# Kernel tuning notes

Measured on AMD Instinct MI355X. Metric: run time of the kernel, lower is better.

Reference implementation:

```python
import jax, jax.numpy as jnp
import numpy as np

B = 16384      # games
BS = 19        # board size
N2 = BS * BS   # 361
G = 8          # groups per board
S = 4          # stones per group
R = B * G      # total groups
K = R * S      # total stones
M = N2         # hash history length (H*W*history_factor)
I32MIN = np.iinfo(np.int32).min
I32MAX = np.iinfo(np.int32).max
NEG = jnp.float32(-1e9)


def setup_inputs() -> dict:
    key = jax.random.key(0)
    ks = jax.random.split(key, 10)
    logits = jax.random.normal(ks[0], (B, BS, BS), dtype=jnp.float32)
    legal_mask = jax.random.uniform(ks[1], (B, BS, BS)) < 0.7
    current_player = jax.random.randint(ks[2], (B,), 0, 2, dtype=jnp.int32)
    current_hash = jax.random.randint(ks[3], (B,), 0, I32MAX, dtype=jnp.int32)
    hash_history = jax.random.randint(ks[4], (B, M), 0, I32MAX, dtype=jnp.int32)
    move_count = jax.random.randint(ks[5], (B,), 0, M, dtype=jnp.int32)
    ZposT = jax.random.randint(ks[6], (3, N2), 0, I32MAX, dtype=jnp.int32)
    stone_global_index = jax.random.randint(ks[7], (K,), 0, N2, dtype=jnp.int32)
    stone_global_pointer = jnp.arange(R + 1, dtype=jnp.int32) * S          # CSR: stones per group
    group_global_pointer_per_board = jnp.arange(B + 1, dtype=jnp.int32) * G  # CSR: groups per board
    cap_idx = jax.random.randint(ks[8], (B, N2, 4), 0, G, dtype=jnp.int32)
    cap_on = jax.random.uniform(ks[9], (B, N2, 4)) < 0.05
    captured_group_local_index = jnp.where(cap_on, cap_idx, jnp.int32(-1))
    return {
        "logits": logits,
        "legal_mask": legal_mask,
        "current_player": current_player,
        "current_hash": current_hash,
        "hash_history": hash_history,
        "move_count": move_count,
        "ZposT": ZposT,
        "stone_global_index": stone_global_index,
        "stone_global_pointer": stone_global_pointer,
        "group_global_pointer_per_board": group_global_pointer_per_board,
        "captured_group_local_index": captured_group_local_index,
    }


def reference(logits, legal_mask, current_player, current_hash, hash_history,
              move_count, ZposT, stone_global_index, stone_global_pointer,
              group_global_pointer_per_board, captured_group_local_index):
    Bn, H, W = legal_mask.shape
    Rn = stone_global_pointer.shape[0] - 1
    Kn = stone_global_index.shape[0]
    z_empty, z_black, z_white = ZposT[0], ZposT[1], ZposT[2]

    # Placement delta: empty -> current player's stone, for every candidate point. (B, N2)
    placement_delta = z_empty[None, :] ^ jnp.where(
        (current_player == 0)[:, None], z_black[None, :], z_white[None, :])

    # Map each group -> board, each stone -> group (CSR expansion).
    groups_per_board = group_global_pointer_per_board[1:] - group_global_pointer_per_board[:-1]
    group_board = jnp.repeat(jnp.arange(Bn, dtype=jnp.int32), groups_per_board,
                             total_repeat_length=Rn)
    stones_per_group = stone_global_pointer[1:] - stone_global_pointer[:-1]
    group_for_stone = jnp.repeat(jnp.arange(Rn, dtype=jnp.int32), stones_per_group,
                                 total_repeat_length=Kn)
    stone_board = group_board[group_for_stone]

    # Per-stone removal delta: opponent stone -> empty.
    opp_for_stone = (1 - current_player)[stone_board]           # (K,)
    si = stone_global_index.astype(jnp.int32)
    z_opp = ZposT[1 + opp_for_stone, si]
    per_stone_delta = z_opp ^ z_empty[si]                        # (K,) int32

    # Segmented XOR reduction over each group's stones via XOR prefix scan.
    prefix = jax.lax.associative_scan(jnp.bitwise_xor, per_stone_delta)
    start = stone_global_pointer[:-1]
    end = stone_global_pointer[1:]
    end_val = prefix[jnp.clip(end - 1, 0)]
    start_val = jnp.where(start > 0, prefix[jnp.clip(start - 1, 0)], jnp.int32(0))
    group_xor = end_val ^ start_val                              # (R,) per-group removal delta

    # Gather capture deltas for up to 4 captured neighbor groups per candidate move.
    offs = group_global_pointer_per_board[:-1][:, None, None]    # (B,1,1)
    flat_ids = jnp.clip(captured_group_local_index, 0) + offs    # (B,N2,4)
    cap_vals = jnp.where(captured_group_local_index >= 0, group_xor[flat_ids], jnp.int32(0))
    capture_delta = cap_vals[..., 0] ^ cap_vals[..., 1] ^ cap_vals[..., 2] ^ cap_vals[..., 3]

    candidate = current_hash[:, None] ^ placement_delta ^ capture_delta  # (B, N2)

    # Super-ko repeat detection against hash history (mask, sort, searchsorted).
    Mh = hash_history.shape[1]
    valid = jnp.arange(Mh, dtype=jnp.int32)[None, :] < jnp.minimum(move_count, Mh)[:, None]
    masked_hist = jnp.where(valid, hash_history, jnp.int32(I32MIN))
    sorted_hist = jnp.sort(masked_hist, axis=1)
    idx = jnp.clip(
        jax.vmap(lambda h, c: jnp.searchsorted(h, c, side='right'))(sorted_hist, candidate) - 1,
        0)
    found = jnp.take_along_axis(sorted_hist, idx, axis=1)
    repeat = (found == candidate).reshape(Bn, H, W)

    final_mask = legal_mask & ~repeat
    return jnp.where(final_mask, logits, NEG)
```

## Files before the change

### kernel.cpp

```cpp
#include <hip/hip_runtime.h>
#include <stdint.h>

#define N2 361
#define BMW 512u
#define EMPTY 0x80000000u
#define NEGV -998244352.0f

__global__ __launch_bounds__(256) void k_groups(
    const int* __restrict__ current_player,
    const int* __restrict__ ZposT,
    const int* __restrict__ stone_global_index,
    const int* __restrict__ stone_global_pointer,
    unsigned*  __restrict__ gx_out,
    const void* __restrict__ legal_raw,
    unsigned*  __restrict__ fmt_out,
    int packed_bits, int Rn)
{
    const int r = blockIdx.x * 256 + threadIdx.x;

    if (blockIdx.x == 0 && threadIdx.x < 64) {
        const int lane = threadIdx.x;
        const unsigned* lwd = (const unsigned*)legal_raw;
        const unsigned dv0 = lwd[lane];
        const unsigned dv1 = (lane < 27) ? lwd[64 + lane] : 0u;
        auto classify = [](unsigned v) -> unsigned {
            unsigned f = 0;
            #pragma unroll
            for (int j = 0; j < 4; ++j) {
                const unsigned bv = (v >> (8 * j)) & 0xFFu;
                if (bv > 1u) f |= 1u;
                if (j != 0 && bv != 0u) f |= 2u;
            }
            const unsigned x = v & 0xFFFFu, y = v >> 16;
            if ((x && x != 0x3F80u) || (y && y != 0x3F80u)) f |= 4u;
            if (x == 0x3F80u) f |= 8u;
            return f;
        };
        unsigned fcl = classify(dv0);
        if (lane < 27) fcl |= classify(dv1);
        unsigned fa = 0;
        fa |= __ballot(fcl & 1u) ? 1u : 0u;
        fa |= __ballot(fcl & 2u) ? 2u : 0u;
        fa |= __ballot(fcl & 4u) ? 4u : 0u;
        fa |= __ballot(fcl & 8u) ? 8u : 0u;
        unsigned fmt;
        if (packed_bits) fmt = 4u;
        else if (!(fa & 1u)) fmt = (fa & 2u) ? 1u : 0u;
        else if (!(fa & 4u)) fmt = (fa & 8u) ? 2u : 0u;
        else fmt = 1u;
        if (lane == 0) fmt_out[0] = fmt;
    }

    if (r < Rn) {
        const int sp0 = stone_global_pointer[r];
        const int sp1 = stone_global_pointer[r + 1];
        const int b   = r >> 3;
        const int cp  = current_player[b];
        const int opprow = (2 - cp) * N2;
        unsigned x = 0u;
        for (int k = sp0; k < sp1; ++k) {
            const int si = stone_global_index[k];
            x ^= (unsigned)ZposT[opprow + si] ^ (unsigned)ZposT[si];
        }
        gx_out[r] = x;
    }
}

__device__ __forceinline__ unsigned sel8(uint4 a, uint4 b, unsigned i) {
    const unsigned r01 = (i & 1u) ? a.y : a.x;
    const unsigned r23 = (i & 1u) ? a.w : a.z;
    const unsigned r45 = (i & 1u) ? b.y : b.x;
    const unsigned r67 = (i & 1u) ? b.w : b.z;
    const unsigned r03 = (i & 2u) ? r23 : r01;
    const unsigned r47 = (i & 2u) ? r67 : r45;
    return (i & 4u) ? r47 : r03;
}

__global__ __launch_bounds__(384) void k_cand(
    const int* __restrict__ current_hash,
    const int* __restrict__ current_player,
    const int* __restrict__ ZposT,
    const int4* __restrict__ captured4,
    const unsigned* __restrict__ gx_ws,
    unsigned* __restrict__ cand_out)
{
    const int b = blockIdx.x;
    const int t = threadIdx.x;
    if (t >= N2) return;
    const unsigned ch = (unsigned)current_hash[b];
    const int cp = current_player[b];
    const uint4 ga = *(const uint4*)(gx_ws + b * 8);
    const uint4 gb = *(const uint4*)(gx_ws + b * 8 + 4);
    const size_t q = (size_t)b * N2 + t;
    const int4 c = captured4[q];
    unsigned capd = 0u;
    if (c.x >= 0) capd ^= sel8(ga, gb, (unsigned)c.x & 7u);
    if (c.y >= 0) capd ^= sel8(ga, gb, (unsigned)c.y & 7u);
    if (c.z >= 0) capd ^= sel8(ga, gb, (unsigned)c.z & 7u);
    if (c.w >= 0) capd ^= sel8(ga, gb, (unsigned)c.w & 7u);
    const int prow = (1 + cp) * N2;
    const unsigned zz = (unsigned)ZposT[t] ^ (unsigned)ZposT[prow + t];
    cand_out[q] = ch ^ zz ^ capd;
}

template <int MODE>
__global__ __launch_bounds__(512) void k_mask(
    const float* __restrict__ logits,
    const void*  __restrict__ legal_raw,
    const int*   __restrict__ move_count,
    const int*   __restrict__ hash_history,
    const unsigned* __restrict__ cand_ws,
    const unsigned* __restrict__ fmt_ws,
    const int*   __restrict__ current_hash,
    const int*   __restrict__ current_player,
    const int*   __restrict__ ZposT,
    const int4*  __restrict__ captured4,
    const unsigned* __restrict__ gx_ws,
    float* __restrict__ out,
    int Btot)
{
    __shared__ unsigned s_bm[8 * BMW];
    const int tid  = threadIdx.x;
    const int wid  = tid >> 6;
    const int lane = tid & 63;
    const int b    = __builtin_amdgcn_readfirstlane(blockIdx.x * 8 + wid);
    if (b >= Btot) return;
    unsigned* bm = s_bm + wid * BMW;
    const size_t bbase = (size_t)b * N2;

    int cnt = move_count[b];
    cnt = cnt < 0 ? 0 : (cnt > N2 ? N2 : cnt);
    const int fmt = (int)fmt_ws[0];

    const int*  hist  = hash_history + bbase;
    const int4* hist4 = (const int4*)hist;
    const int4  ha    = hist4[lane];
    const int4  hb    = (lane < 26) ? hist4[64 + lane] : int4{0, 0, 0, 0};
    const int   hc    = (lane == 26) ? hist[360] : 0;

    unsigned cand[6];
    if (MODE == 0) {
        #pragma unroll
        for (int s = 0; s < 6; ++s) {
            const int n = lane + 64 * s;
            cand[s] = cand_ws[bbase + ((n < N2) ? n : (N2 - 1))];
        }
    } else {
        const unsigned ch = (unsigned)current_hash[b];
        const int cp = current_player[b];
        const int prow = (1 + cp) * N2;
        const uint4 ga = *(const uint4*)(gx_ws + b * 8);
        const uint4 gb2 = *(const uint4*)(gx_ws + b * 8 + 4);
        #pragma unroll
        for (int s = 0; s < 6; ++s) {
            const int n  = lane + 64 * s;
            const int nc = (n < N2) ? n : (N2 - 1);
            const int4 c = captured4[bbase + nc];
            unsigned capd = 0u;
            if (c.x >= 0) capd ^= sel8(ga, gb2, (unsigned)c.x & 7u);
            if (c.y >= 0) capd ^= sel8(ga, gb2, (unsigned)c.y & 7u);
            if (c.z >= 0) capd ^= sel8(ga, gb2, (unsigned)c.z & 7u);
            if (c.w >= 0) capd ^= sel8(ga, gb2, (unsigned)c.w & 7u);
            cand[s] = ch ^ (unsigned)ZposT[nc] ^ (unsigned)ZposT[prow + nc] ^ capd;
        }
    }

    float lg[6]; unsigned leg[6];
    #pragma unroll
    for (int s = 0; s < 6; ++s) {
        const int n = lane + 64 * s;
        const size_t q = bbase + ((n < N2) ? n : (N2 - 1));
        lg[s] = logits[q];
        if (fmt == 0)      leg[s] = ((const unsigned*)legal_raw)[q];
        else if (fmt == 1) leg[s] = ((const uint8_t*)legal_raw)[q];
        else if (fmt == 2) leg[s] = ((const uint16_t*)legal_raw)[q];
        else               leg[s] = (((const uint8_t*)legal_raw)[q >> 3] >> (q & 7)) & 1u;
    }

    {
        uint4* t4 = (uint4*)bm;
        const uint4 z4 = {0u, 0u, 0u, 0u};
        t4[lane] = z4;
        t4[64 + lane] = z4;
    }

    const int i0 = 4 * lane, i1 = 256 + 4 * lane;
    const unsigned e0 = (i0 + 0 < cnt) ? (unsigned)ha.x : EMPTY;
    const unsigned e1 = (i0 + 1 < cnt) ? (unsigned)ha.y : EMPTY;
    const unsigned e2 = (i0 + 2 < cnt) ? (unsigned)ha.z : EMPTY;
    const unsigned e3 = (i0 + 3 < cnt) ? (unsigned)ha.w : EMPTY;
    const unsigned e4 = (lane < 26 && i1 + 0 < cnt) ? (unsigned)hb.x : EMPTY;
    const unsigned e5 = (lane < 26 && i1 + 1 < cnt) ? (unsigned)hb.y : EMPTY;
    const unsigned e6 = (lane < 26 && i1 + 2 < cnt) ? (unsigned)hb.z : EMPTY;
    const unsigned e7 = (lane < 26 && i1 + 3 < cnt) ? (unsigned)hb.w : EMPTY;
    const unsigned e8 = (lane == 26 && 360 < cnt)   ? (unsigned)hc   : EMPTY;

    asm volatile("s_waitcnt lgkmcnt(0)" ::: "memory");
    __builtin_amdgcn_sched_barrier(0);

    auto setbit = [&](unsigned v) {
        if (!(v & EMPTY)) atomicOr(&bm[(v >> 5) & (BMW - 1u)], 1u << (v & 31u));
    };
    setbit(e0); setbit(e1); setbit(e2); setbit(e3);
    setbit(e4); setbit(e5); setbit(e6); setbit(e7); setbit(e8);

    asm volatile("s_waitcnt lgkmcnt(0)" ::: "memory");
    __builtin_amdgcn_sched_barrier(0);

    unsigned bw[6];
    #pragma unroll
    for (int s = 0; s < 6; ++s) bw[s] = bm[(cand[s] >> 5) & (BMW - 1u)];

    auto match9 = [&](unsigned c) -> bool {
        return (e0 == c) | (e1 == c) | (e2 == c) | (e3 == c) |
               (e4 == c) | (e5 == c) | (e6 == c) | (e7 == c) | (e8 == c);
    };

    #pragma unroll
    for (int s = 0; s < 6; ++s) {
        const int n = lane + 64 * s;
        const bool inr = n < N2;
        bool rep = false;
        unsigned long long mask = __ballot(inr && ((bw[s] >> (cand[s] & 31u)) & 1u));
        while (mask) {
            const int l = __ffsll((unsigned long long)mask) - 1;
            const unsigned c = (unsigned)__shfl((int)cand[s], l);
            const unsigned long long fm = __ballot(match9(c));
            if (lane == l) rep = (fm != 0ull);
            mask &= mask - 1;
        }
        if (inr) {
            const float v = (leg[s] && !rep) ? lg[s] : NEGV;
            __builtin_nontemporal_store(v, &out[bbase + n]);
        }
    }
}

extern "C" void kernel_launch(void* const* d_in, const int* in_sizes, int n_in,
                              void* d_out, int out_size, void* d_ws, size_t ws_size,
                              hipStream_t stream) {
    const float* logits  = (const float*)d_in[0];
    const void*  legal   = (const void*)d_in[1];
    const int*   cur_pl  = (const int*)d_in[2];
    const int*   cur_h   = (const int*)d_in[3];
    const int*   hist    = (const int*)d_in[4];
    const int*   mcount  = (const int*)d_in[5];
    const int*   zpos    = (const int*)d_in[6];
    const int*   sgi     = (const int*)d_in[7];
    const int*   sgp     = (const int*)d_in[8];
    const int4*  cap4    = (const int4*)d_in[10];
    float*       out     = (float*)d_out;

    const int B  = in_sizes[2];
    const int Rn = in_sizes[8] - 1;
    const int packed = (in_sizes[1] != in_sizes[0]);

    const size_t fmt_off  = (size_t)Rn * 4;
    const size_t cand_off = ((fmt_off + 4 + 255) / 256) * 256;
    const size_t need_full = cand_off + (size_t)B * N2 * 4;

    unsigned* gx_ws   = (unsigned*)d_ws;
    unsigned* fmt_ws  = (unsigned*)((char*)d_ws + fmt_off);
    unsigned* cand_ws = (unsigned*)((char*)d_ws + cand_off);

    k_groups<<<(Rn + 255) / 256, 256, 0, stream>>>(
        cur_pl, zpos, sgi, sgp, gx_ws, legal, fmt_ws, packed, Rn);

    const int mask_blocks = (B + 7) / 8;
    if (ws_size >= need_full) {
        k_cand<<<B, 384, 0, stream>>>(cur_h, cur_pl, zpos, cap4, gx_ws, cand_ws);
        k_mask<0><<<mask_blocks, 512, 0, stream>>>(
            logits, legal, mcount, hist, cand_ws, fmt_ws,
            cur_h, cur_pl, zpos, cap4, gx_ws, out, B);
    } else {
        k_mask<1><<<mask_blocks, 512, 0, stream>>>(
            logits, legal, mcount, hist, cand_ws, fmt_ws,
            cur_h, cur_pl, zpos, cap4, gx_ws, out, B);
    }
}
```

Baseline: 229.5 us.

## Fuse candidate-hash computation into mask kernel and enlarge shared bitmap

Removes the separate k_cand kernel and its workspace round-trip, so candidate hashes are computed inside the mask kernel. Capture indices, logits, Zobrist values and legal bits are all loaded up front, and the capture XOR math runs while the LDS atomics that build the history bitmap are in flight. The per-board bitmap doubles from 512 to 1024 words, which lowers false-positive bucket hits at the cost of twice the shared memory per block. The bounds check on b is dropped, which assumes B is a multiple of 8.

```diff
diff --git a/kernel.cpp b/kernel.cpp
--- a/kernel.cpp
+++ b/kernel.cpp
@@ -2,7 +2,7 @@
 #include <stdint.h>
 
 #define N2 361
-#define BMW 512u
+#define BMW 1024u
 #define EMPTY 0x80000000u
 #define NEGV -998244352.0f
 
@@ -76,112 +76,64 @@
     return (i & 4u) ? r47 : r03;
 }
 
-__global__ __launch_bounds__(384) void k_cand(
-    const int* __restrict__ current_hash,
-    const int* __restrict__ current_player,
-    const int* __restrict__ ZposT,
-    const int4* __restrict__ captured4,
-    const unsigned* __restrict__ gx_ws,
-    unsigned* __restrict__ cand_out)
-{
-    const int b = blockIdx.x;
-    const int t = threadIdx.x;
-    if (t >= N2) return;
-    const unsigned ch = (unsigned)current_hash[b];
-    const int cp = current_player[b];
-    const uint4 ga = *(const uint4*)(gx_ws + b * 8);
-    const uint4 gb = *(const uint4*)(gx_ws + b * 8 + 4);
-    const size_t q = (size_t)b * N2 + t;
-    const int4 c = captured4[q];
-    unsigned capd = 0u;
-    if (c.x >= 0) capd ^= sel8(ga, gb, (unsigned)c.x & 7u);
-    if (c.y >= 0) capd ^= sel8(ga, gb, (unsigned)c.y & 7u);
-    if (c.z >= 0) capd ^= sel8(ga, gb, (unsigned)c.z & 7u);
-    if (c.w >= 0) capd ^= sel8(ga, gb, (unsigned)c.w & 7u);
-    const int prow = (1 + cp) * N2;
-    const unsigned zz = (unsigned)ZposT[t] ^ (unsigned)ZposT[prow + t];
-    cand_out[q] = ch ^ zz ^ capd;
-}
-
-template <int MODE>
-__global__ __launch_bounds__(512) void k_mask(
+__global__ __launch_bounds__(512) void k_main(
     const float* __restrict__ logits,
     const void*  __restrict__ legal_raw,
-    const int*   __restrict__ move_count,
-    const int*   __restrict__ hash_history,
-    const unsigned* __restrict__ cand_ws,
-    const unsigned* __restrict__ fmt_ws,
     const int*   __restrict__ current_hash,
     const int*   __restrict__ current_player,
+    const int*   __restrict__ hash_history,
+    const int*   __restrict__ move_count,
     const int*   __restrict__ ZposT,
     const int4*  __restrict__ captured4,
     const unsigned* __restrict__ gx_ws,
-    float* __restrict__ out,
-    int Btot)
+    const unsigned* __restrict__ fmt_ws,
+    float* __restrict__ out)
 {
     __shared__ unsigned s_bm[8 * BMW];
     const int tid  = threadIdx.x;
     const int wid  = tid >> 6;
     const int lane = tid & 63;
     const int b    = __builtin_amdgcn_readfirstlane(blockIdx.x * 8 + wid);
-    if (b >= Btot) return;
-    unsigned* bm = s_bm + wid * BMW;
+    unsigned* bm   = s_bm + wid * BMW;
     const size_t bbase = (size_t)b * N2;
 
     int cnt = move_count[b];
     cnt = cnt < 0 ? 0 : (cnt > N2 ? N2 : cnt);
-    const int fmt = (int)fmt_ws[0];
+    const int      fmt = (int)fmt_ws[0];
+    const unsigned ch  = (unsigned)current_hash[b];
+    const int      cp  = current_player[b];
+    const uint4    ga  = *(const uint4*)(gx_ws + b * 8);
+    const uint4    gb  = *(const uint4*)(gx_ws + b * 8 + 4);
+    const int      prow = (1 + cp) * N2;
 
     const int*  hist  = hash_history + bbase;
     const int4* hist4 = (const int4*)hist;
     const int4  ha    = hist4[lane];
-    const int4  hb    = (lane < 26) ? hist4[64 + lane] : int4{0, 0, 0, 0};
+    const int4  hb    = (lane < 26) ? hist4[64 + lane] : int4{0,0,0,0};
     const int   hc    = (lane == 26) ? hist[360] : 0;
 
-    unsigned cand[6];
-    if (MODE == 0) {
-        #pragma unroll
-        for (int s = 0; s < 6; ++s) {
-            const int n = lane + 64 * s;
-            cand[s] = cand_ws[bbase + ((n < N2) ? n : (N2 - 1))];
-        }
-    } else {
-        const unsigned ch = (unsigned)current_hash[b];
-        const int cp = current_player[b];
-        const int prow = (1 + cp) * N2;
-        const uint4 ga = *(const uint4*)(gx_ws + b * 8);
-        const uint4 gb2 = *(const uint4*)(gx_ws + b * 8 + 4);
-        #pragma unroll
-        for (int s = 0; s < 6; ++s) {
-            const int n  = lane + 64 * s;
-            const int nc = (n < N2) ? n : (N2 - 1);
-            const int4 c = captured4[bbase + nc];
-            unsigned capd = 0u;
-            if (c.x >= 0) capd ^= sel8(ga, gb2, (unsigned)c.x & 7u);
-            if (c.y >= 0) capd ^= sel8(ga, gb2, (unsigned)c.y & 7u);
-            if (c.z >= 0) capd ^= sel8(ga, gb2, (unsigned)c.z & 7u);
-            if (c.w >= 0) capd ^= sel8(ga, gb2, (unsigned)c.w & 7u);
-            cand[s] = ch ^ (unsigned)ZposT[nc] ^ (unsigned)ZposT[prow + nc] ^ capd;
-        }
-    }
-
-    float lg[6]; unsigned leg[6];
+    int4 cap[6]; float lg[6]; unsigned zz[6]; unsigned leg[6];
     #pragma unroll
     for (int s = 0; s < 6; ++s) {
-        const int n = lane + 64 * s;
-        const size_t q = bbase + ((n < N2) ? n : (N2 - 1));
-        lg[s] = logits[q];
+        const int n  = lane + 64 * s;
+        const int nc = (n < N2) ? n : (N2 - 1);
+        const size_t q = bbase + nc;
+        cap[s] = captured4[q];
+        lg[s]  = logits[q];
+        zz[s]  = (unsigned)ZposT[nc] ^ (unsigned)ZposT[prow + nc];
         if (fmt == 0)      leg[s] = ((const unsigned*)legal_raw)[q];
         else if (fmt == 1) leg[s] = ((const uint8_t*)legal_raw)[q];
         else if (fmt == 2) leg[s] = ((const uint16_t*)legal_raw)[q];
         else               leg[s] = (((const uint8_t*)legal_raw)[q >> 3] >> (q & 7)) & 1u;
     }
 
+    asm volatile("" ::: "memory");
+
     {
         uint4* t4 = (uint4*)bm;
         const uint4 z4 = {0u, 0u, 0u, 0u};
-        t4[lane] = z4;
-        t4[64 + lane] = z4;
+        #pragma unroll
+        for (int i = 0; i < 4; ++i) t4[lane + 64 * i] = z4;
     }
 
     const int i0 = 4 * lane, i1 = 256 + 4 * lane;
@@ -203,6 +155,18 @@
     };
     setbit(e0); setbit(e1); setbit(e2); setbit(e3);
     setbit(e4); setbit(e5); setbit(e6); setbit(e7); setbit(e8);
+
+    unsigned cand[6];
+    #pragma unroll
+    for (int s = 0; s < 6; ++s) {
+        unsigned capd = 0u;
+        const int4 c = cap[s];
+        if (c.x >= 0) capd ^= sel8(ga, gb, (unsigned)c.x & 7u);
+        if (c.y >= 0) capd ^= sel8(ga, gb, (unsigned)c.y & 7u);
+        if (c.z >= 0) capd ^= sel8(ga, gb, (unsigned)c.z & 7u);
+        if (c.w >= 0) capd ^= sel8(ga, gb, (unsigned)c.w & 7u);
+        cand[s] = ch ^ zz[s] ^ capd;
+    }
 
     asm volatile("s_waitcnt lgkmcnt(0)" ::: "memory");
     __builtin_amdgcn_sched_barrier(0);
@@ -255,26 +219,13 @@
     const int Rn = in_sizes[8] - 1;
     const int packed = (in_sizes[1] != in_sizes[0]);
 
-    const size_t fmt_off  = (size_t)Rn * 4;
-    const size_t cand_off = ((fmt_off + 4 + 255) / 256) * 256;
-    const size_t need_full = cand_off + (size_t)B * N2 * 4;
-
-    unsigned* gx_ws   = (unsigned*)d_ws;
-    unsigned* fmt_ws  = (unsigned*)((char*)d_ws + fmt_off);
-    unsigned* cand_ws = (unsigned*)((char*)d_ws + cand_off);
+    unsigned* gx_ws  = (unsigned*)d_ws;
+    unsigned* fmt_ws = (unsigned*)((char*)d_ws + (size_t)Rn * 4);
 
     k_groups<<<(Rn + 255) / 256, 256, 0, stream>>>(
         cur_pl, zpos, sgi, sgp, gx_ws, legal, fmt_ws, packed, Rn);
 
-    const int mask_blocks = (B + 7) / 8;
-    if (ws_size >= need_full) {
-        k_cand<<<B, 384, 0, stream>>>(cur_h, cur_pl, zpos, cap4, gx_ws, cand_ws);
-        k_mask<0><<<mask_blocks, 512, 0, stream>>>(
-            logits, legal, mcount, hist, cand_ws, fmt_ws,
-            cur_h, cur_pl, zpos, cap4, gx_ws, out, B);
-    } else {
-        k_mask<1><<<mask_blocks, 512, 0, stream>>>(
-            logits, legal, mcount, hist, cand_ws, fmt_ws,
-            cur_h, cur_pl, zpos, cap4, gx_ws, out, B);
-    }
-}
+    k_main<<<B / 8, 512, 0, stream>>>(
+        logits, legal, cur_h, cur_pl, hist, mcount, zpos,
+        cap4, gx_ws, fmt_ws, out);
+}
```

Measured after the change: 223.9 us. 2.4% less time.
